# Optimization experiments

Measured on AMD Instinct MI355X. Metric: run time of the kernel, lower is better.

## Reference

```python
import jax, jax.numpy as jnp
import numpy as np

B, C_IN, C_OUT, C_KEY, N = 8, 512, 512, 256, 2048


def setup_inputs() -> dict:
    key = jax.random.key(0)
    k1, k2, k3, k4 = jax.random.split(key, 4)
    x = jax.random.normal(k1, (B, C_IN, N), dtype=jnp.float32)
    # Conv1d(kernel=1, bias=False) weights -> plain linear maps over channel dim
    Wq = jax.random.normal(k2, (C_KEY, C_IN), dtype=jnp.float32) * (1.0 / np.sqrt(C_IN))
    Wk = jax.random.normal(k3, (C_KEY, C_IN), dtype=jnp.float32) * (1.0 / np.sqrt(C_IN))
    Wv = jax.random.normal(k4, (C_OUT, C_IN), dtype=jnp.float32) * (1.0 / np.sqrt(C_IN))
    return {"x": x, "Wq": Wq, "Wk": Wk, "Wv": Wv}


def reference(x, Wq, Wk, Wv):
    # 1x1 conv projections: [B, C, N] -> [B, Ck/Co, N]
    q = jnp.einsum("oc,bcn->bon", Wq, x)
    k = jnp.einsum("oc,bcn->bon", Wk, x)
    v = jnpqv = jnp.einsum("oc,bcn->bon", Wv, x)
    # sim_map[b,i,j] = sum_c k[b,c,i] * q[b,c,j]  (unscaled)
    sim = jnp.einsum("bci,bcj->bij", k, q)  # [B, N, N]
    attn = jax.nn.softmax(sim, axis=-1)
    # out = value @ sim_map, then permute(0,2,1) -> [B, N, C_out]
    out = jnp.einsum("bck,bkm->bmc", jnpqv, attn)
    return out
```

## Files before the change

### kernel.cpp

```cpp
#include <hip/hip_runtime.h>

typedef _Float16 half8 __attribute__((ext_vector_type(8)));
typedef _Float16 half4v __attribute__((ext_vector_type(4)));
typedef _Float16 half2v __attribute__((ext_vector_type(2)));
typedef float f32x4 __attribute__((ext_vector_type(4)));

#define ASYNC_CP16(gp, lp)                                       \
  __builtin_amdgcn_global_load_lds(                              \
      (const __attribute__((address_space(1))) void*)(gp),       \
      (__attribute__((address_space(3))) void*)(lp), 16, 0, 0)

__global__ __launch_bounds__(256) void conv_w(const float* __restrict__ Wq,
                                              const float* __restrict__ Wk,
                                              const float* __restrict__ Wv,
                                              _Float16* __restrict__ Wb) {
  int idx = blockIdx.x * 256 + threadIdx.x;
  int row = idx >> 9;
  float v;
  if (row < 256)      v = Wq[idx];
  else if (row < 512) v = Wk[idx - 256 * 512];
  else                v = Wv[idx - 512 * 512];
  Wb[idx] = (_Float16)v;
}

__global__ __launch_bounds__(256) void conv_xT(const float* __restrict__ x,
                                               _Float16* __restrict__ xT) {
  __shared__ float T[32][33];
  const int b = blockIdx.z;
  const int n0 = blockIdx.x * 32, c0 = blockIdx.y * 32;
  const int t = threadIdx.x;
  const float* xb = x + (size_t)b * 512 * 2048;
  const int n2 = t & 15, cr = t >> 4;
#pragma unroll
  for (int r = 0; r < 2; r++) {
    int c = cr + r * 16;
    float2 v = *(const float2*)&xb[(size_t)(c0 + c) * 2048 + n0 + n2 * 2];
    T[c][n2 * 2] = v.x;
    T[c][n2 * 2 + 1] = v.y;
  }
  __syncthreads();
  _Float16* xtb = xT + (size_t)b * 2048 * 512;
  const int c2 = t & 15, nr = t >> 4;
#pragma unroll
  for (int r = 0; r < 2; r++) {
    int n = nr + r * 16;
    half2v h;
    h[0] = (_Float16)T[c2 * 2][n];
    h[1] = (_Float16)T[c2 * 2 + 1][n];
    *(half2v*)&xtb[(size_t)(n0 + n) * 512 + c0 + c2 * 2] = h;
  }
}

template <typename OutT, int BUFS, int MODE>
__global__ __launch_bounds__(256) void gemm_nt(
    const _Float16* __restrict__ A, const _Float16* __restrict__ B,
    OutT* __restrict__ C, OutT* __restrict__ C2, int K, int lda, int ldb,
    int ldc, int ldc2, long sA, long sB, long sC, float* __restrict__ pm,
    float* __restrict__ ps) {
  A += (size_t)blockIdx.z * sA;
  B += (size_t)blockIdx.z * sB;
  C += (size_t)blockIdx.z * sC;
  if constexpr (MODE == 1) C2 += (size_t)blockIdx.z * sC;
  const int m_blk = blockIdx.y * 128, n_blk = blockIdx.x * 128;

  __shared__ _Float16 As[BUFS][4096];
  __shared__ _Float16 Bs[BUFS][4096];

  const int t = threadIdx.x;
  const int lane = t & 63, wave = t >> 6;
  const int quad = lane >> 4, l16 = lane & 15;
  const int wm = (wave & 1) * 64, wn = (wave >> 1) * 64;

  const int srow = 16 * wave + (lane >> 2);
  const int schunk = (lane & 3) ^ ((lane >> 3) & 3);
  const _Float16* gA0 = A + (size_t)(m_blk + srow) * lda + schunk * 8;
  const _Float16* gA1 = gA0 + (size_t)64 * lda;
  const _Float16* gB0 = B + (size_t)(n_blk + srow) * ldb + schunk * 8;
  const _Float16* gB1 = gB0 + (size_t)64 * ldb;
  const int lofs = wave * 512 + lane * 8;

  const int rchunk = (quad ^ ((l16 >> 1) & 3)) * 8;

  f32x4 acc[4][4] = {};

#pragma unroll
  for (int pb = 0; pb < BUFS - 1; pb++) {
    if (pb * 32 < K) {
      ASYNC_CP16(gA0 + pb * 32, &As[pb][lofs]);
      ASYNC_CP16(gA1 + pb * 32, &As[pb][lofs + 2048]);
      ASYNC_CP16(gB0 + pb * 32, &Bs[pb][lofs]);
      ASYNC_CP16(gB1 + pb * 32, &Bs[pb][lofs + 2048]);
    }
  }

  int ib = 0;
  for (int k0 = 0; k0 < K; k0 += 32) {
    if constexpr (BUFS == 3) {
      if (k0 + 32 < K)
        asm volatile("s_waitcnt vmcnt(4)\n\ts_barrier" ::: "memory");
      else
        asm volatile("s_waitcnt vmcnt(0)\n\ts_barrier" ::: "memory");
    } else {
      asm volatile("s_waitcnt vmcnt(0)\n\ts_barrier" ::: "memory");
    }
    if (k0 + (BUFS - 1) * 32 < K) {
      int nb = ib + BUFS - 1;
      if (nb >= BUFS) nb -= BUFS;
      const int ko = k0 + (BUFS - 1) * 32;
      ASYNC_CP16(gA0 + ko, &As[nb][lofs]);
      ASYNC_CP16(gA1 + ko, &As[nb][lofs + 2048]);
      ASYNC_CP16(gB0 + ko, &Bs[nb][lofs]);
      ASYNC_CP16(gB1 + ko, &Bs[nb][lofs + 2048]);
    }
    half8 af[4], bf[4];
#pragma unroll
    for (int i = 0; i < 4; i++) {
      af[i] = *(const half8*)&As[ib][(wm + i * 16 + l16) * 32 + rchunk];
      bf[i] = *(const half8*)&Bs[ib][(wn + i * 16 + l16) * 32 + rchunk];
    }
#pragma unroll
    for (int i = 0; i < 4; i++)
#pragma unroll
      for (int j = 0; j < 4; j++)
        acc[i][j] =
            __builtin_amdgcn_mfma_f32_16x16x32_f16(af[i], bf[j], acc[i][j], 0, 0, 0);
    ib++;
    if (ib == BUFS) ib = 0;
  }

#pragma unroll
  for (int i = 0; i < 4; i++) {
    const int m0 = m_blk + wm + i * 16 + quad * 4;
#pragma unroll
    for (int j = 0; j < 4; j++) {
      const int n0 = n_blk + wn + j * 16 + l16;
      if constexpr (MODE == 1) {
        if (m_blk < 512) {
          half4v h;
#pragma unroll
          for (int r = 0; r < 4; r++) h[r] = (_Float16)acc[i][j][r];
          *(half4v*)&C[(size_t)n0 * ldc + m0] = h;
        } else {
#pragma unroll
          for (int r = 0; r < 4; r++)
            C2[(size_t)(m0 - 512 + r) * ldc2 + n0] = (OutT)acc[i][j][r];
        }
      } else if constexpr (MODE == 2) {
#pragma unroll
        for (int r = 0; r < 4; r++) {
          _Float16 h = (_Float16)acc[i][j][r];
          C[(size_t)(m0 + r) * ldc + n0] = h;
          acc[i][j][r] = (float)h;
        }
      } else {
#pragma unroll
        for (int r = 0; r < 4; r++)
          C[(size_t)(m0 + r) * ldc + n0] = (OutT)acc[i][j][r];
      }
    }
  }

  if constexpr (MODE == 2) {
    __shared__ float sred[128][2][2];
    float pM[4], pS[4];
#pragma unroll
    for (int j = 0; j < 4; j++) {
      float mx = acc[0][j][0];
#pragma unroll
      for (int i = 0; i < 4; i++)
#pragma unroll
        for (int r = 0; r < 4; r++) mx = fmaxf(mx, acc[i][j][r]);
      mx = fmaxf(mx, __shfl_xor(mx, 16, 64));
      mx = fmaxf(mx, __shfl_xor(mx, 32, 64));
      float es = 0.f;
#pragma unroll
      for (int i = 0; i < 4; i++)
#pragma unroll
        for (int r = 0; r < 4; r++) es += __expf(acc[i][j][r] - mx);
      es += __shfl_xor(es, 16, 64);
      es += __shfl_xor(es, 32, 64);
      pM[j] = mx;
      pS[j] = es;
    }
    if (quad == 0) {
#pragma unroll
      for (int j = 0; j < 4; j++) {
        sred[wn + j * 16 + l16][wave & 1][0] = pM[j];
        sred[wn + j * 16 + l16][wave & 1][1] = pS[j];
      }
    }
    __syncthreads();
    if (t < 128) {
      float m0 = sred[t][0][0], s0 = sred[t][0][1];
      float m1 = sred[t][1][0], s1 = sred[t][1][1];
      float M = fmaxf(m0, m1);
      float S = s0 * __expf(m0 - M) + s1 * __expf(m1 - M);
      size_t o = ((size_t)blockIdx.z * 16 + blockIdx.y) * 2048 + n_blk + t;
      pm[o] = M;
      ps[o] = S;
    }
  }
}

__global__ __launch_bounds__(256) void colstats2(const float* __restrict__ pm,
                                                 const float* __restrict__ ps,
                                                 float* __restrict__ shift) {
  const int idx = blockIdx.x * 256 + threadIdx.x;
  const int b = idx >> 11, col = idx & 2047;
  const float* pmb = pm + (size_t)b * 16 * 2048 + col;
  const float* psb = ps + (size_t)b * 16 * 2048 + col;
  float m = -3.0e38f;
#pragma unroll
  for (int i = 0; i < 16; i++) m = fmaxf(m, pmb[(size_t)i * 2048]);
  float s = 0.f;
#pragma unroll
  for (int i = 0; i < 16; i++)
    s += psb[(size_t)i * 2048] * __expf(pmb[(size_t)i * 2048] - m);
  shift[idx] = m + __logf(s);
}

__global__ __launch_bounds__(256) void gemm_av(const _Float16* __restrict__ A,
                                               const _Float16* __restrict__ V,
                                               const float* __restrict__ shift,
                                               float* __restrict__ C,
                                               int cbatch) {
  int lin = blockIdx.x, z, idx;
  if (cbatch == 8) {
    z = lin & 7;
    idx = lin >> 3;
  } else {
    z = lin >> 6;
    idx = lin & 63;
  }
  const int n_blk = (idx & 3) * 128;
  const int m_blk = (idx >> 2) * 128;
  A += (size_t)z * 2048 * 2048;
  V += (size_t)z * 512 * 2048;
  shift += (size_t)z * 2048;
  C += (size_t)z * 2048 * 512;

  __shared__ _Float16 As[2][4096];
  __shared__ _Float16 Bs[2][4096];

  const int t = threadIdx.x;
  const int lane = t & 63, wave = t >> 6;
  const int quad = lane >> 4, l16 = lane & 15;
  const int wm = (wave & 1) * 64, wn = (wave >> 1) * 64;

  const int srow = 16 * wave + (lane >> 2);
  const int schunk = (lane & 3) ^ ((lane >> 3) & 3);
  const _Float16* gA0 = A + (size_t)(m_blk + srow) * 2048 + schunk * 8;
  const _Float16* gA1 = gA0 + (size_t)64 * 2048;
  const _Float16* gB0 = V + (size_t)(n_blk + srow) * 2048 + schunk * 8;
  const _Float16* gB1 = gB0 + (size_t)64 * 2048;
  const float* gS = shift + schunk * 8;
  const int lofs = wave * 512 + lane * 8;
  const int rchunk = (quad ^ ((l16 >> 1) & 3)) * 8;

  f32x4 acc[4][4] = {};

  auto expw = [](half8 a, f32x4 s0, f32x4 s1) -> half8 {
    half8 o;
#pragma unroll
    for (int j = 0; j < 4; j++) {
      o[j] = (_Float16)__expf((float)a[j] - s0[j]);
      o[j + 4] = (_Float16)__expf((float)a[j + 4] - s1[j]);
    }
    return o;
  };

  ASYNC_CP16(gB0, &Bs[0][lofs]);
  ASYNC_CP16(gB1, &Bs[0][lofs + 2048]);
  {
    half8 a0 = *(const half8*)gA0;
    half8 a1 = *(const half8*)gA1;
    f32x4 s0 = *(const f32x4*)gS;
    f32x4 s1 = *(const f32x4*)(gS + 4);
    *(half8*)&As[0][lofs] = expw(a0, s0, s1);
    *(half8*)&As[0][lofs + 2048] = expw(a1, s0, s1);
  }
  __syncthreads();

  int ib = 0;
  for (int k0 = 0; k0 < 2048; k0 += 32, ib ^= 1) {
    half8 a0, a1;
    f32x4 s0, s1;
    const bool more = (k0 + 32 < 2048);
    if (more) {
      ASYNC_CP16(gB0 + k0 + 32, &Bs[ib ^ 1][lofs]);
      ASYNC_CP16(gB1 + k0 + 32, &Bs[ib ^ 1][lofs + 2048]);
      a0 = *(const half8*)(gA0 + k0 + 32);
      a1 = *(const half8*)(gA1 + k0 + 32);
      s0 = *(const f32x4*)(gS + k0 + 32);
      s1 = *(const f32x4*)(gS + k0 + 36);
    }
    half8 af[4], bf[4];
#pragma unroll
    for (int i = 0; i < 4; i++) {
      af[i] = *(const half8*)&As[ib][(wm + i * 16 + l16) * 32 + rchunk];
      bf[i] = *(const half8*)&Bs[ib][(wn + i * 16 + l16) * 32 + rchunk];
    }
#pragma unroll
    for (int i = 0; i < 4; i++)
#pragma unroll
      for (int j = 0; j < 4; j++)
        acc[i][j] =
            __builtin_amdgcn_mfma_f32_16x16x32_f16(af[i], bf[j], acc[i][j], 0, 0, 0);
    if (more) {
      *(half8*)&As[ib ^ 1][lofs] = expw(a0, s0, s1);
      *(half8*)&As[ib ^ 1][lofs + 2048] = expw(a1, s0, s1);
    }
    __syncthreads();
  }

#pragma unroll
  for (int i = 0; i < 4; i++) {
    const int m0 = m_blk + wm + i * 16 + quad * 4;
#pragma unroll
    for (int j = 0; j < 4; j++) {
      const int n0 = n_blk + wn + j * 16 + l16;
#pragma unroll
      for (int r = 0; r < 4; r++) C[(size_t)(m0 + r) * 512 + n0] = acc[i][j][r];
    }
  }
}

extern "C" void kernel_launch(void* const* d_in, const int* in_sizes, int n_in,
                              void* d_out, int out_size, void* d_ws,
                              size_t ws_size, hipStream_t stream) {
  const float* x = (const float*)d_in[0];
  const float* Wq = (const float*)d_in[1];
  const float* Wk = (const float*)d_in[2];
  const float* Wv = (const float*)d_in[3];
  float* out = (float*)d_out;

  char* p = (char*)d_ws;
  auto alloc = [&](size_t bytes) -> char* {
    char* r = p;
    p += (bytes + 255) & ~(size_t)255;
    return r;
  };
  const size_t NB = 8, N = 2048, CIN = 512, CO = 512;
  _Float16* Wb = (_Float16*)alloc(1024 * 512 * sizeof(_Float16));
  _Float16* xT = (_Float16*)alloc(NB * N * CIN * sizeof(_Float16));
  _Float16* qkT = (_Float16*)alloc(NB * N * 512 * sizeof(_Float16));
  _Float16* v = (_Float16*)alloc(NB * CO * N * sizeof(_Float16));
  size_t base_used = (size_t)(p - (char*)d_ws);

  const size_t per_b = (size_t)N * N * 2 + 2 * 16 * N * 4 + N * 4 + 8192;
  int cb = 8;
  while (cb > 1 && base_used + (size_t)cb * per_b > ws_size) cb >>= 1;
  _Float16* simH = (_Float16*)alloc((size_t)cb * N * N * 2);
  float* pm = (float*)alloc((size_t)cb * 16 * N * 4);
  float* ps = (float*)alloc((size_t)cb * 16 * N * 4);
  float* shift = (float*)alloc((size_t)cb * N * 4);

  conv_w<<<dim3(1024 * 512 / 256), 256, 0, stream>>>(Wq, Wk, Wv, Wb);
  conv_xT<<<dim3(64, 16, 8), 256, 0, stream>>>(x, xT);

  gemm_nt<_Float16, 3, 1><<<dim3(16, 8, 8), 256, 0, stream>>>(
      Wb, xT, qkT, v, 512, 512, 512, 512, 2048, 0, (long)(N * CIN),
      (long)(N * 512), nullptr, nullptr);

  for (int b0 = 0; b0 < 8; b0 += cb) {
    const _Float16* qT = qkT + (size_t)b0 * N * 512;
    const _Float16* kT = qkT + (size_t)b0 * N * 512 + 256;
    gemm_nt<_Float16, 2, 2><<<dim3(16, 16, cb), 256, 0, stream>>>(
        qT, kT, simH, nullptr, 256, 512, 512, 2048, 0, (long)(N * 512),
        (long)(N * 512), (long)(N * N), pm, ps);
    colstats2<<<dim3(cb * 8), 256, 0, stream>>>(pm, ps, shift);
    gemm_av<<<dim3(64 * cb), 256, 0, stream>>>(
        simH, v + (size_t)b0 * CO * N, shift, out + (size_t)b0 * N * CO, cb);
  }
}
```

Baseline: 225.5 us.

## Store local-max exp in sim GEMM; rescale with fp16 multipliers in AV GEMM

The similarity GEMM epilogue now writes exp(s - local 64-row max) in fp16 instead of raw logits, and records per-wave max and sum directly, so the shared-memory reduction and its barrier are gone. colstats2 combines 32 partials per column and emits fp16 per-block scale factors, which already include the 1/sum normalisation. The AV GEMM then only multiplies by those scales instead of running an exp per element. The AV B operand also moves to a three-stage prefetch with a hand-written waitcnt and barrier. This removes transcendental work from the AV inner loop and deepens load pipelining, at the cost of more partial-stat traffic and fp16 precision risk in the rescaled values.

```diff
diff --git a/kernel.cpp b/kernel.cpp
--- a/kernel.cpp
+++ b/kernel.cpp
@@ -9,6 +9,13 @@
   __builtin_amdgcn_global_load_lds(                              \
       (const __attribute__((address_space(1))) void*)(gp),       \
       (__attribute__((address_space(3))) void*)(lp), 16, 0, 0)
+
+static __device__ __forceinline__ half8 mulw(half8 a, half8 s) {
+  half8 o;
+#pragma unroll
+  for (int j = 0; j < 8; j++) o[j] = a[j] * s[j];
+  return o;
+}
 
 __global__ __launch_bounds__(256) void conv_w(const float* __restrict__ Wq,
                                               const float* __restrict__ Wk,
@@ -128,43 +135,10 @@
     if (ib == BUFS) ib = 0;
   }
 
-#pragma unroll
-  for (int i = 0; i < 4; i++) {
-    const int m0 = m_blk + wm + i * 16 + quad * 4;
+  if constexpr (MODE == 2) {
 #pragma unroll
     for (int j = 0; j < 4; j++) {
       const int n0 = n_blk + wn + j * 16 + l16;
-      if constexpr (MODE == 1) {
-        if (m_blk < 512) {
-          half4v h;
-#pragma unroll
-          for (int r = 0; r < 4; r++) h[r] = (_Float16)acc[i][j][r];
-          *(half4v*)&C[(size_t)n0 * ldc + m0] = h;
-        } else {
-#pragma unroll
-          for (int r = 0; r < 4; r++)
-            C2[(size_t)(m0 - 512 + r) * ldc2 + n0] = (OutT)acc[i][j][r];
-        }
-      } else if constexpr (MODE == 2) {
-#pragma unroll
-        for (int r = 0; r < 4; r++) {
-          _Float16 h = (_Float16)acc[i][j][r];
-          C[(size_t)(m0 + r) * ldc + n0] = h;
-          acc[i][j][r] = (float)h;
-        }
-      } else {
-#pragma unroll
-        for (int r = 0; r < 4; r++)
-          C[(size_t)(m0 + r) * ldc + n0] = (OutT)acc[i][j][r];
-      }
-    }
-  }
-
-  if constexpr (MODE == 2) {
-    __shared__ float sred[128][2][2];
-    float pM[4], pS[4];
-#pragma unroll
-    for (int j = 0; j < 4; j++) {
       float mx = acc[0][j][0];
 #pragma unroll
       for (int i = 0; i < 4; i++)
@@ -174,54 +148,81 @@
       mx = fmaxf(mx, __shfl_xor(mx, 32, 64));
       float es = 0.f;
 #pragma unroll
-      for (int i = 0; i < 4; i++)
-#pragma unroll
-        for (int r = 0; r < 4; r++) es += __expf(acc[i][j][r] - mx);
+      for (int i = 0; i < 4; i++) {
+        const int m0 = m_blk + wm + i * 16 + quad * 4;
+#pragma unroll
+        for (int r = 0; r < 4; r++) {
+          _Float16 h = (_Float16)__expf(acc[i][j][r] - mx);
+          C[(size_t)(m0 + r) * ldc + n0] = h;
+          es += (float)h;
+        }
+      }
       es += __shfl_xor(es, 16, 64);
       es += __shfl_xor(es, 32, 64);
-      pM[j] = mx;
-      pS[j] = es;
-    }
-    if (quad == 0) {
+      if (quad == 0) {
+        size_t o =
+            ((size_t)blockIdx.z * 32 + blockIdx.y * 2 + (wave & 1)) * 2048 + n0;
+        pm[o] = mx;
+        ps[o] = es;
+      }
+    }
+  } else {
+#pragma unroll
+    for (int i = 0; i < 4; i++) {
+      const int m0 = m_blk + wm + i * 16 + quad * 4;
 #pragma unroll
       for (int j = 0; j < 4; j++) {
-        sred[wn + j * 16 + l16][wave & 1][0] = pM[j];
-        sred[wn + j * 16 + l16][wave & 1][1] = pS[j];
+        const int n0 = n_blk + wn + j * 16 + l16;
+        if constexpr (MODE == 1) {
+          if (m_blk < 512) {
+            half4v h;
+#pragma unroll
+            for (int r = 0; r < 4; r++) h[r] = (_Float16)acc[i][j][r];
+            *(half4v*)&C[(size_t)n0 * ldc + m0] = h;
+          } else {
+#pragma unroll
+            for (int r = 0; r < 4; r++)
+              C2[(size_t)(m0 - 512 + r) * ldc2 + n0] = (OutT)acc[i][j][r];
+          }
+        } else {
+#pragma unroll
+          for (int r = 0; r < 4; r++)
+            C[(size_t)(m0 + r) * ldc + n0] = (OutT)acc[i][j][r];
+        }
       }
-    }
-    __syncthreads();
-    if (t < 128) {
-      float m0 = sred[t][0][0], s0 = sred[t][0][1];
-      float m1 = sred[t][1][0], s1 = sred[t][1][1];
-      float M = fmaxf(m0, m1);
-      float S = s0 * __expf(m0 - M) + s1 * __expf(m1 - M);
-      size_t o = ((size_t)blockIdx.z * 16 + blockIdx.y) * 2048 + n_blk + t;
-      pm[o] = M;
-      ps[o] = S;
     }
   }
 }
 
 __global__ __launch_bounds__(256) void colstats2(const float* __restrict__ pm,
                                                  const float* __restrict__ ps,
-                                                 float* __restrict__ shift) {
+                                                 _Float16* __restrict__ scl) {
   const int idx = blockIdx.x * 256 + threadIdx.x;
   const int b = idx >> 11, col = idx & 2047;
-  const float* pmb = pm + (size_t)b * 16 * 2048 + col;
-  const float* psb = ps + (size_t)b * 16 * 2048 + col;
+  const float* pmb = pm + (size_t)b * 32 * 2048 + col;
+  const float* psb = ps + (size_t)b * 32 * 2048 + col;
+  float pv[32];
   float m = -3.0e38f;
 #pragma unroll
-  for (int i = 0; i < 16; i++) m = fmaxf(m, pmb[(size_t)i * 2048]);
+  for (int i = 0; i < 32; i++) {
+    pv[i] = pmb[(size_t)i * 2048];
+    m = fmaxf(m, pv[i]);
+  }
   float s = 0.f;
 #pragma unroll
-  for (int i = 0; i < 16; i++)
-    s += psb[(size_t)i * 2048] * __expf(pmb[(size_t)i * 2048] - m);
-  shift[idx] = m + __logf(s);
-}
-
-__global__ __launch_bounds__(256) void gemm_av(const _Float16* __restrict__ A,
+  for (int i = 0; i < 32; i++) {
+    pv[i] = __expf(pv[i] - m);
+    s += psb[(size_t)i * 2048] * pv[i];
+  }
+  const float inv = 1.0f / s;
+  _Float16* so = scl + (size_t)b * 32 * 2048 + col;
+#pragma unroll
+  for (int i = 0; i < 32; i++) so[(size_t)i * 2048] = (_Float16)(pv[i] * inv);
+}
+
+__global__ __launch_bounds__(256) void gemm_av(const _Float16* __restrict__ P,
                                                const _Float16* __restrict__ V,
-                                               const float* __restrict__ shift,
+                                               const _Float16* __restrict__ scl,
                                                float* __restrict__ C,
                                                int cbatch) {
   int lin = blockIdx.x, z, idx;
@@ -234,13 +235,13 @@
   }
   const int n_blk = (idx & 3) * 128;
   const int m_blk = (idx >> 2) * 128;
-  A += (size_t)z * 2048 * 2048;
+  P += (size_t)z * 2048 * 2048;
   V += (size_t)z * 512 * 2048;
-  shift += (size_t)z * 2048;
+  scl += ((size_t)z * 32 + (m_blk >> 6)) * 2048;
   C += (size_t)z * 2048 * 512;
 
   __shared__ _Float16 As[2][4096];
-  __shared__ _Float16 Bs[2][4096];
+  __shared__ _Float16 Bs[3][4096];
 
   const int t = threadIdx.x;
   const int lane = t & 63, wave = t >> 6;
@@ -249,56 +250,56 @@
 
   const int srow = 16 * wave + (lane >> 2);
   const int schunk = (lane & 3) ^ ((lane >> 3) & 3);
-  const _Float16* gA0 = A + (size_t)(m_blk + srow) * 2048 + schunk * 8;
+  const _Float16* gA0 = P + (size_t)(m_blk + srow) * 2048 + schunk * 8;
   const _Float16* gA1 = gA0 + (size_t)64 * 2048;
   const _Float16* gB0 = V + (size_t)(n_blk + srow) * 2048 + schunk * 8;
   const _Float16* gB1 = gB0 + (size_t)64 * 2048;
-  const float* gS = shift + schunk * 8;
+  const _Float16* gS0 = scl + schunk * 8;
+  const _Float16* gS1 = gS0 + 2048;
   const int lofs = wave * 512 + lane * 8;
   const int rchunk = (quad ^ ((l16 >> 1) & 3)) * 8;
 
   f32x4 acc[4][4] = {};
 
-  auto expw = [](half8 a, f32x4 s0, f32x4 s1) -> half8 {
-    half8 o;
-#pragma unroll
-    for (int j = 0; j < 4; j++) {
-      o[j] = (_Float16)__expf((float)a[j] - s0[j]);
-      o[j + 4] = (_Float16)__expf((float)a[j + 4] - s1[j]);
-    }
-    return o;
-  };
-
   ASYNC_CP16(gB0, &Bs[0][lofs]);
   ASYNC_CP16(gB1, &Bs[0][lofs + 2048]);
+  ASYNC_CP16(gB0 + 32, &Bs[1][lofs]);
+  ASYNC_CP16(gB1 + 32, &Bs[1][lofs + 2048]);
   {
     half8 a0 = *(const half8*)gA0;
     half8 a1 = *(const half8*)gA1;
-    f32x4 s0 = *(const f32x4*)gS;
-    f32x4 s1 = *(const f32x4*)(gS + 4);
-    *(half8*)&As[0][lofs] = expw(a0, s0, s1);
-    *(half8*)&As[0][lofs + 2048] = expw(a1, s0, s1);
-  }
+    half8 s0 = *(const half8*)gS0;
+    half8 s1 = *(const half8*)gS1;
+    *(half8*)&As[0][lofs] = mulw(a0, s0);
+    *(half8*)&As[0][lofs + 2048] = mulw(a1, s1);
+  }
+  half8 an0 = *(const half8*)(gA0 + 32);
+  half8 an1 = *(const half8*)(gA1 + 32);
+  half8 sn0 = *(const half8*)(gS0 + 32);
+  half8 sn1 = *(const half8*)(gS1 + 32);
   __syncthreads();
 
-  int ib = 0;
-  for (int k0 = 0; k0 < 2048; k0 += 32, ib ^= 1) {
-    half8 a0, a1;
-    f32x4 s0, s1;
-    const bool more = (k0 + 32 < 2048);
-    if (more) {
-      ASYNC_CP16(gB0 + k0 + 32, &Bs[ib ^ 1][lofs]);
-      ASYNC_CP16(gB1 + k0 + 32, &Bs[ib ^ 1][lofs + 2048]);
-      a0 = *(const half8*)(gA0 + k0 + 32);
-      a1 = *(const half8*)(gA1 + k0 + 32);
-      s0 = *(const f32x4*)(gS + k0 + 32);
-      s1 = *(const f32x4*)(gS + k0 + 36);
+  int ibA = 0, ibB = 0;
+  for (int k0 = 0; k0 < 2048; k0 += 32) {
+    const bool m1 = (k0 + 32 < 2048), m2 = (k0 + 64 < 2048);
+    if (m2) {
+      int nb = ibB + 2;
+      if (nb >= 3) nb -= 3;
+      ASYNC_CP16(gB0 + k0 + 64, &Bs[nb][lofs]);
+      ASYNC_CP16(gB1 + k0 + 64, &Bs[nb][lofs + 2048]);
+    }
+    half8 a20, a21, s20, s21;
+    if (m2) {
+      a20 = *(const half8*)(gA0 + k0 + 64);
+      a21 = *(const half8*)(gA1 + k0 + 64);
+      s20 = *(const half8*)(gS0 + k0 + 64);
+      s21 = *(const half8*)(gS1 + k0 + 64);
     }
     half8 af[4], bf[4];
 #pragma unroll
     for (int i = 0; i < 4; i++) {
-      af[i] = *(const half8*)&As[ib][(wm + i * 16 + l16) * 32 + rchunk];
-      bf[i] = *(const half8*)&Bs[ib][(wn + i * 16 + l16) * 32 + rchunk];
+      af[i] = *(const half8*)&As[ibA][(wm + i * 16 + l16) * 32 + rchunk];
+      bf[i] = *(const half8*)&Bs[ibB][(wn + i * 16 + l16) * 32 + rchunk];
     }
 #pragma unroll
     for (int i = 0; i < 4; i++)
@@ -306,11 +307,20 @@
       for (int j = 0; j < 4; j++)
         acc[i][j] =
             __builtin_amdgcn_mfma_f32_16x16x32_f16(af[i], bf[j], acc[i][j], 0, 0, 0);
-    if (more) {
-      *(half8*)&As[ib ^ 1][lofs] = expw(a0, s0, s1);
-      *(half8*)&As[ib ^ 1][lofs + 2048] = expw(a1, s0, s1);
-    }
-    __syncthreads();
+    if (m1) {
+      *(half8*)&As[ibA ^ 1][lofs] = mulw(an0, sn0);
+      *(half8*)&As[ibA ^ 1][lofs + 2048] = mulw(an1, sn1);
+      if (m2) {
+        an0 = a20;
+        an1 = a21;
+        sn0 = s20;
+        sn1 = s21;
+      }
+      asm volatile("s_waitcnt vmcnt(6) lgkmcnt(0)\n\ts_barrier" ::: "memory");
+    }
+    ibA ^= 1;
+    ibB++;
+    if (ibB == 3) ibB = 0;
   }
 
 #pragma unroll
@@ -347,13 +357,14 @@
   _Float16* v = (_Float16*)alloc(NB * CO * N * sizeof(_Float16));
   size_t base_used = (size_t)(p - (char*)d_ws);
 
-  const size_t per_b = (size_t)N * N * 2 + 2 * 16 * N * 4 + N * 4 + 8192;
+  const size_t per_b =
+      (size_t)N * N * 2 + 2 * 32 * N * 4 + 32 * N * 2 + 8192;
   int cb = 8;
   while (cb > 1 && base_used + (size_t)cb * per_b > ws_size) cb >>= 1;
   _Float16* simH = (_Float16*)alloc((size_t)cb * N * N * 2);
-  float* pm = (float*)alloc((size_t)cb * 16 * N * 4);
-  float* ps = (float*)alloc((size_t)cb * 16 * N * 4);
-  float* shift = (float*)alloc((size_t)cb * N * 4);
+  float* pm = (float*)alloc((size_t)cb * 32 * N * 4);
+  float* ps = (float*)alloc((size_t)cb * 32 * N * 4);
+  _Float16* scl = (_Float16*)alloc((size_t)cb * 32 * N * 2);
 
   conv_w<<<dim3(1024 * 512 / 256), 256, 0, stream>>>(Wq, Wk, Wv, Wb);
   conv_xT<<<dim3(64, 16, 8), 256, 0, stream>>>(x, xT);
@@ -368,8 +379,8 @@
     gemm_nt<_Float16, 2, 2><<<dim3(16, 16, cb), 256, 0, stream>>>(
         qT, kT, simH, nullptr, 256, 512, 512, 2048, 0, (long)(N * 512),
         (long)(N * 512), (long)(N * N), pm, ps);
-    colstats2<<<dim3(cb * 8), 256, 0, stream>>>(pm, ps, shift);
+    colstats2<<<dim3(cb * 8), 256, 0, stream>>>(pm, ps, scl);
     gemm_av<<<dim3(64 * cb), 256, 0, stream>>>(
-        simH, v + (size_t)b0 * CO * N, shift, out + (size_t)b0 * N * CO, cb);
-  }
-}
+        simH, v + (size_t)b0 * CO * N, scl, out + (size_t)b0 * N * CO, cb);
+  }
+}
```

After: 211.1 us. 6.4% less time.
